# Kernel tuning notes

Hardware: AMD Instinct MI355X
Metric: run time of the kernel (lower is better)

## Reference

```python
import jax, jax.numpy as jnp
import numpy as np

H = 4096  # grid height
W = 4096  # grid width


def setup_inputs() -> dict:
    key = jax.random.key(0)
    k1, k2 = jax.random.split(key)
    x = jax.random.normal(k1, (H,), dtype=jnp.float32)
    # xavier_uniform with fan_in=3, fan_out=3 => bound = sqrt(6/(3+3)) = 1.0
    bound = float(np.sqrt(6.0 / (3.0 + 3.0)))
    w = jax.random.uniform(k2, (H, W), dtype=jnp.float32, minval=-bound, maxval=bound)
    b = jnp.zeros((H, W), dtype=jnp.float32)
    return {"x": x, "w": w, "b": b}


def _shift_down(a, k):
    # prepend k zero rows / elements along axis 0, drop last k
    pad_shape = (k,) + a.shape[1:]
    return jnp.concatenate([jnp.zeros(pad_shape, a.dtype), a[: a.shape[0] - k]], axis=0)


def reference(x, w, b):
    # The torch module zero-pads w (one row top/bottom) and keeps activation
    # rows 0 and H+1 at zero. The 3-tap stencil a[i-1],a[i],a[i+1] (padded idx)
    # for output row i reduces, in unpadded coords, to:
    #   z[i] = c[i-2]*w[i-2] + c[i-1]*w[i-1] + c[i]*w[i] + b[i]
    # with zero boundary for negative indices.
    Hh, Ww = b.shape
    wm2 = _shift_down(w, 2)  # w[i-2] with zero boundary, (H, W)
    wm1 = _shift_down(w, 1)  # w[i-1]
    # scan across columns (width); carry the activation column (H,)
    xs = (wm2.T, wm1.T, w.T, b.T)  # each (W, H)

    def step(col, ws):
        a2, a1, a0, bj = ws
        z = _shift_down(col, 2) * a2 + _shift_down(col, 1) * a1 + col * a0 + bj
        new = jnp.sin(z)
        return new, None

    final, _ = jax.lax.scan(step, x.reshape(Hh), xs)
    return final.reshape(1, Hh)
```

## Files before the change

### kernel.cpp

```cpp
#include <hip/hip_runtime.h>
#include <math.h>

#define HH 4096
#define WW 4096
#define NB 64
#define U 8
#define NGR (WW / U)
#define GATE 64


__device__ __forceinline__ unsigned long long halo_ld(unsigned long long* p) {
    return __hip_atomic_load(p, __ATOMIC_RELAXED, __HIP_MEMORY_SCOPE_AGENT);
}
__device__ __forceinline__ void halo_st(unsigned long long* p, unsigned long long v) {
    __hip_atomic_store(p, v, __ATOMIC_RELAXED, __HIP_MEMORY_SCOPE_AGENT);
}

__device__ __forceinline__ float f4c(const float4& v, int k) {
    return (k == 0) ? v.x : ((k == 1) ? v.y : ((k == 2) ? v.z : v.w));
}

__device__ __forceinline__ float wave_shr1(float src, float fill) {
    return __int_as_float(__builtin_amdgcn_update_dpp(
        __float_as_int(fill), __float_as_int(src), 0x138, 0xF, 0xF, false));
}

__device__ __forceinline__ float fast_sin(float z) {
    return __builtin_amdgcn_sinf(z * 0.15915494309189535f);
}

#define COLSTEP(M, K)                                                        \
    do {                                                                     \
        float am1 = wave_shr1(a, Hhi[M][K]);                                 \
        float am2 = wave_shr1(am1, Hlo[M][K]);                               \
        const float z = fmaf(am2, f4c(W2v[M][(K) >> 2], (K) & 3),            \
                        fmaf(am1, f4c(W1v[M][(K) >> 2], (K) & 3),            \
                        fmaf(a,   f4c(Wv[M][(K) >> 2],  (K) & 3),            \
                                  f4c(Bv[M][(K) >> 2],  (K) & 3))));         \
        a = fast_sin(z);                                                     \
        Pv[K] = a;                    \
    } while (0)

#define PUBG(JB)                                                             \
    do {                                                                     \
        float pv = 0.0f;                                                     \
        _Pragma("unroll")                                                    \
        for (int k = 0; k < U; ++k) {                                        \
            float t = __shfl(Pv[k], 62 + (lane & 1));                        \
            if ((lane >> 1) == k) pv = t;                                    \
        }                                                                    \
        const int e = (JB) + 1 + (lane >> 1);                                \
        if (lane < 16 && e < WW) {                                           \
            unsigned long long v =                                           \
                ((unsigned long long)(unsigned)(e + 1) << 32) |              \
                (unsigned long long)__float_as_uint(pv);                     \
            halo_st(&hme[(size_t)e * 2 + (lane & 1)], v);                    \
        }                                                                    \
    } while (0)

#define LOADW(M, J)                                                          \
    do {                                                                     \
        const int _j = (J);                                                  \
        Wv[M][0]  = *(const float4*)(wp  + _j);                              \
        Wv[M][1]  = *(const float4*)(wp  + _j + 4);                          \
        W1v[M][0] = *(const float4*)(wp1 + _j);                              \
        W1v[M][1] = *(const float4*)(wp1 + _j + 4);                          \
        W2v[M][0] = *(const float4*)(wp2 + _j);                              \
        W2v[M][1] = *(const float4*)(wp2 + _j + 4);                          \
        Bv[M][0]  = *(const float4*)(bp  + _j);                              \
        Bv[M][1]  = *(const float4*)(bp  + _j + 4);                          \
    } while (0)

#define UNPACKG(GIDX, BUF, SLOT)                                             \
    do {                                                                     \
        const int _jn = (GIDX) * U;                                          \
        if (blk > 0) {                                                       \
            bool myok = (lane >= 16) ||                                      \
                ((unsigned)(Hg[SLOT] >> 32) ==                               \
                 (unsigned)(_jn + (lane >> 1) + 1));                         \
            if (__builtin_expect(!__all(myok), 0)) {                         \
                for (;;) {                                                   \
                    if (lane < 16)                                           \
                        Hg[SLOT] = halo_ld(&hsrc[(size_t)_jn * 2 + lane]);   \
                    myok = (lane >= 16) ||                                   \
                        ((unsigned)(Hg[SLOT] >> 32) ==                       \
                         (unsigned)(_jn + (lane >> 1) + 1));                 \
                    if (__all(myok)) break;                                  \
                    __builtin_amdgcn_s_sleep(2);                             \
                }                                                            \
            }                                                                \
            float _hv = __uint_as_float((unsigned)(Hg[SLOT] & 0xffffffffu)); \
            _Pragma("unroll")                                                \
            for (int k = 0; k < U; ++k) {                                    \
                Hlo[BUF][k] = __shfl(_hv, 2 * k);                            \
                Hhi[BUF][k] = __shfl(_hv, 2 * k + 1);                        \
            }                                                                \
        }                                                                    \
    } while (0)

#define GROUPBODY(S)                                                         \
    do {                                                                     \
        const int G  = g4 * 4 + (S);                                         \
        const int jb = G * U;                                                \
        if (G + 1 < NGR) UNPACKG(G + 1, ((S) + 1) & 1, ((S) + 1) & 3);       \
        _Pragma("unroll")                                                    \
        for (int k = 0; k < U; ++k) COLSTEP((S) & 1, k);                     \
        PUBG(jb);                                                            \
        const int jw = jb + 2 * U;                                           \
        if (jw < WW) LOADW((S) & 1, jw);                                     \
        const int jh = jb + 4 * U;                                           \
        if (jh < WW && blk > 0 && lane < 16)                                 \
            Hg[S] = halo_ld(&hsrc[(size_t)jh * 2 + lane]);                   \
    } while (0)

__global__ __launch_bounds__(64, 1) void neural_grid_scan(
    const float* __restrict__ x, const float* __restrict__ w,
    const float* __restrict__ bb, float* __restrict__ out,
    unsigned long long* __restrict__ halo)
{
    const int lane = threadIdx.x;
    const int blk  = blockIdx.x;
    const int row  = blk * 64 + lane;
    const int r1 = (row >= 1) ? row - 1 : 0;
    const int r2 = (row >= 2) ? row - 2 : 0;

    const float* wp  = w  + (size_t)row * WW;
    const float* wp1 = w  + (size_t)r1  * WW;
    const float* wp2 = w  + (size_t)r2  * WW;
    const float* bp  = bb + (size_t)row * WW;

    unsigned long long* hme  = halo + (size_t)blk * WW * 2;
    unsigned long long* hsrc = halo + (size_t)(blk - 1) * WW * 2;

    float a = x[row];

    if (lane >= 62) {
        unsigned long long v = (1ULL << 32) | (unsigned long long)__float_as_uint(a);
        halo_st(&hme[lane - 62], v);
    }

    if (blk > 0 && lane == 0) {
        while ((unsigned)(halo_ld(&hsrc[(size_t)GATE * 2]) >> 32)
               != (unsigned)(GATE + 1)) {
            __builtin_amdgcn_s_sleep(8);
        }
    }

    float4 Wv[2][2], W1v[2][2], W2v[2][2], Bv[2][2];
    unsigned long long Hg[4];
    float Hlo[2][U] = {}, Hhi[2][U] = {};
    float Pv[U];

    LOADW(0, 0);
    LOADW(1, U);
    if (blk > 0 && lane < 16) {
        Hg[0] = halo_ld(&hsrc[(size_t)(0 * U) * 2 + lane]);
        Hg[1] = halo_ld(&hsrc[(size_t)(1 * U) * 2 + lane]);
        Hg[2] = halo_ld(&hsrc[(size_t)(2 * U) * 2 + lane]);
        Hg[3] = halo_ld(&hsrc[(size_t)(3 * U) * 2 + lane]);
    } else {
        Hg[0] = Hg[1] = Hg[2] = Hg[3] = 0;
    }
    UNPACKG(0, 0, 0);

    for (int g4 = 0; g4 < NGR / 4; ++g4) {
        GROUPBODY(0);
        GROUPBODY(1);
        GROUPBODY(2);
        GROUPBODY(3);
    }

    out[row] = a;
}

extern "C" void kernel_launch(void* const* d_in, const int* in_sizes, int n_in,
                              void* d_out, int out_size, void* d_ws, size_t ws_size,
                              hipStream_t stream) {
    const float* x = (const float*)d_in[0];
    const float* w = (const float*)d_in[1];
    const float* b = (const float*)d_in[2];
    float* out = (float*)d_out;
    unsigned long long* halo = (unsigned long long*)d_ws;
    neural_grid_scan<<<dim3(NB), dim3(64), 0, stream>>>(x, w, b, out, halo);
}
```

Before: 918.9 us.

## Batch halo polling to 32 columns per full-wave load and raise gate

Halo values from the upstream block are now fetched one 32-column batch at a time, with all 64 lanes each loading one entry, replacing per-8-column loads by 16 lanes. Readiness is checked once per batch instead of once per group, which cuts polling and the cross-lane vote work. The next batch is prefetched one batch ahead. The startup gate is raised so blocks lag further behind their producers, which lowers the chance of stalling on a batch that is not yet ready. The cost is a longer startup skew across the block chain and a dependency on data 32 columns ahead.

```diff
diff --git a/kernel.cpp b/kernel.cpp
--- a/kernel.cpp
+++ b/kernel.cpp
@@ -6,7 +6,8 @@
 #define NB 64
 #define U 8
 #define NGR (WW / U)
-#define GATE 64
+#define NBATCH (WW / 32)
+#define GATE 80
 
 
 __device__ __forceinline__ unsigned long long halo_ld(unsigned long long* p) {
@@ -71,46 +72,49 @@
         Bv[M][1]  = *(const float4*)(bp  + _j + 4);                          \
     } while (0)
 
-#define UNPACKG(GIDX, BUF, SLOT)                                             \
+#define LOADBATCH(DST, M)                                                    \
     do {                                                                     \
-        const int _jn = (GIDX) * U;                                          \
+        if (blk > 0) DST = halo_ld(&hsrc[(size_t)(M) * 64 + lane]);          \
+    } while (0)
+
+#define CHECKBATCH(REG, M)                                                   \
+    do {                                                                     \
         if (blk > 0) {                                                       \
-            bool myok = (lane >= 16) ||                                      \
-                ((unsigned)(Hg[SLOT] >> 32) ==                               \
-                 (unsigned)(_jn + (lane >> 1) + 1));                         \
-            if (__builtin_expect(!__all(myok), 0)) {                         \
+            bool ok = ((unsigned)((REG) >> 32) ==                            \
+                       (unsigned)(32 * (M) + (lane >> 1) + 1));              \
+            if (__builtin_expect(!__all(ok), 0)) {                           \
                 for (;;) {                                                   \
-                    if (lane < 16)                                           \
-                        Hg[SLOT] = halo_ld(&hsrc[(size_t)_jn * 2 + lane]);   \
-                    myok = (lane >= 16) ||                                   \
-                        ((unsigned)(Hg[SLOT] >> 32) ==                       \
-                         (unsigned)(_jn + (lane >> 1) + 1));                 \
-                    if (__all(myok)) break;                                  \
+                    REG = halo_ld(&hsrc[(size_t)(M) * 64 + lane]);           \
+                    ok = ((unsigned)((REG) >> 32) ==                         \
+                          (unsigned)(32 * (M) + (lane >> 1) + 1));           \
+                    if (__all(ok)) break;                                    \
                     __builtin_amdgcn_s_sleep(2);                             \
                 }                                                            \
-            }                                                                \
-            float _hv = __uint_as_float((unsigned)(Hg[SLOT] & 0xffffffffu)); \
-            _Pragma("unroll")                                                \
-            for (int k = 0; k < U; ++k) {                                    \
-                Hlo[BUF][k] = __shfl(_hv, 2 * k);                            \
-                Hhi[BUF][k] = __shfl(_hv, 2 * k + 1);                        \
             }                                                                \
         }                                                                    \
     } while (0)
 
-#define GROUPBODY(S)                                                         \
+#define UNPACKB(REG, I, BUF)                                                 \
     do {                                                                     \
-        const int G  = g4 * 4 + (S);                                         \
-        const int jb = G * U;                                                \
-        if (G + 1 < NGR) UNPACKG(G + 1, ((S) + 1) & 1, ((S) + 1) & 3);       \
+        if (blk > 0) {                                                       \
+            float _hv = __uint_as_float((unsigned)((REG) & 0xffffffffu));    \
+            _Pragma("unroll")                                                \
+            for (int k = 0; k < U; ++k) {                                    \
+                Hlo[BUF][k] = __shfl(_hv, 16 * (I) + 2 * k);                 \
+                Hhi[BUF][k] = __shfl(_hv, 16 * (I) + 2 * k + 1);             \
+            }                                                                \
+        }                                                                    \
+    } while (0)
+
+#define GB(S)                                                                \
+    do {                                                                     \
+        const int jb = (4 * m + (S)) * U;                                    \
+        if ((S) < 3) UNPACKB(Hga, (S) + 1, ((S) + 1) & 1);                   \
         _Pragma("unroll")                                                    \
         for (int k = 0; k < U; ++k) COLSTEP((S) & 1, k);                     \
         PUBG(jb);                                                            \
         const int jw = jb + 2 * U;                                           \
         if (jw < WW) LOADW((S) & 1, jw);                                     \
-        const int jh = jb + 4 * U;                                           \
-        if (jh < WW && blk > 0 && lane < 16)                                 \
-            Hg[S] = halo_ld(&hsrc[(size_t)jh * 2 + lane]);                   \
     } while (0)
 
 __global__ __launch_bounds__(64, 1) void neural_grid_scan(
@@ -147,27 +151,28 @@
     }
 
     float4 Wv[2][2], W1v[2][2], W2v[2][2], Bv[2][2];
-    unsigned long long Hg[4];
     float Hlo[2][U] = {}, Hhi[2][U] = {};
     float Pv[U];
+    unsigned long long Hga = 0, Hgb = 0;
 
     LOADW(0, 0);
     LOADW(1, U);
-    if (blk > 0 && lane < 16) {
-        Hg[0] = halo_ld(&hsrc[(size_t)(0 * U) * 2 + lane]);
-        Hg[1] = halo_ld(&hsrc[(size_t)(1 * U) * 2 + lane]);
-        Hg[2] = halo_ld(&hsrc[(size_t)(2 * U) * 2 + lane]);
-        Hg[3] = halo_ld(&hsrc[(size_t)(3 * U) * 2 + lane]);
-    } else {
-        Hg[0] = Hg[1] = Hg[2] = Hg[3] = 0;
-    }
-    UNPACKG(0, 0, 0);
+    LOADBATCH(Hga, 0);
+    CHECKBATCH(Hga, 0);
+    LOADBATCH(Hgb, 1);
+    UNPACKB(Hga, 0, 0);
 
-    for (int g4 = 0; g4 < NGR / 4; ++g4) {
-        GROUPBODY(0);
-        GROUPBODY(1);
-        GROUPBODY(2);
-        GROUPBODY(3);
+    for (int m = 0; m < NBATCH; ++m) {
+        GB(0);
+        GB(1);
+        GB(2);
+        GB(3);
+        if (m + 1 < NBATCH) {
+            CHECKBATCH(Hgb, m + 1);
+            Hga = Hgb;
+            if (m + 2 < NBATCH) LOADBATCH(Hgb, m + 2);
+            UNPACKB(Hga, 0, 0);
+        }
     }
 
     out[row] = a;
```

Result: slower. 972.6 us (+5.8%).

## Chain waves inside 512-thread blocks via LDS ring halos instead of global

Applied to the files above, without the earlier changes.

Switches from 64 single-wave blocks to 8 blocks of 8 waves. Within a block, neighbouring waves pass their boundary activations through per-wave LDS ring buffers, and a progress counter throttles each producer so it cannot overwrite ring slots before the consumer has read them. Only the first and last waves use the global-memory halo exchange. The goal is to cut the cross-CU atomic latency on the wavefront-pipeline critical path, at the cost of sharing CUs and adding flow-control spinning inside the block.

```diff
diff --git a/kernel.cpp b/kernel.cpp
--- a/kernel.cpp
+++ b/kernel.cpp
@@ -3,10 +3,14 @@
 
 #define HH 4096
 #define WW 4096
-#define NB 64
+#define NB 8
+#define BT 512
 #define U 8
 #define NGR (WW / U)
+#define RING_E 512
+#define RMASK (RING_E - 1)
 #define GATE 64
+#define LGATE 32
 
 
 __device__ __forceinline__ unsigned long long halo_ld(unsigned long long* p) {
@@ -14,6 +18,18 @@
 }
 __device__ __forceinline__ void halo_st(unsigned long long* p, unsigned long long v) {
     __hip_atomic_store(p, v, __ATOMIC_RELAXED, __HIP_MEMORY_SCOPE_AGENT);
+}
+__device__ __forceinline__ unsigned long long lds_ld(const unsigned long long* p) {
+    return __hip_atomic_load(p, __ATOMIC_RELAXED, __HIP_MEMORY_SCOPE_WORKGROUP);
+}
+__device__ __forceinline__ void lds_st(unsigned long long* p, unsigned long long v) {
+    __hip_atomic_store(p, v, __ATOMIC_RELAXED, __HIP_MEMORY_SCOPE_WORKGROUP);
+}
+__device__ __forceinline__ unsigned prog_ld(const unsigned* p) {
+    return __hip_atomic_load(p, __ATOMIC_RELAXED, __HIP_MEMORY_SCOPE_WORKGROUP);
+}
+__device__ __forceinline__ void prog_st(unsigned* p, unsigned v) {
+    __hip_atomic_store(p, v, __ATOMIC_RELAXED, __HIP_MEMORY_SCOPE_WORKGROUP);
 }
 
 __device__ __forceinline__ float f4c(const float4& v, int k) {
@@ -38,23 +54,40 @@
                         fmaf(a,   f4c(Wv[M][(K) >> 2],  (K) & 3),            \
                                   f4c(Bv[M][(K) >> 2],  (K) & 3))));         \
         a = fast_sin(z);                                                     \
-        Pv[K] = a;                    \
-    } while (0)
-
-#define PUBG(JB)                                                             \
-    do {                                                                     \
-        float pv = 0.0f;                                                     \
+        Pv[K] = a;                                                           \
+    } while (0)
+
+#define PACKPV(PVOUT)                                                        \
+    do {                                                                     \
+        PVOUT = 0.0f;                                                        \
         _Pragma("unroll")                                                    \
         for (int k = 0; k < U; ++k) {                                        \
             float t = __shfl(Pv[k], 62 + (lane & 1));                        \
-            if ((lane >> 1) == k) pv = t;                                    \
-        }                                                                    \
+            if ((lane >> 1) == k) PVOUT = t;                                 \
+        }                                                                    \
+    } while (0)
+
+#define PUBG(JB)                                                             \
+    do {                                                                     \
+        float pv; PACKPV(pv);                                                \
         const int e = (JB) + 1 + (lane >> 1);                                \
         if (lane < 16 && e < WW) {                                           \
             unsigned long long v =                                           \
                 ((unsigned long long)(unsigned)(e + 1) << 32) |              \
                 (unsigned long long)__float_as_uint(pv);                     \
             halo_st(&hme[(size_t)e * 2 + (lane & 1)], v);                    \
+        }                                                                    \
+    } while (0)
+
+#define LDSPUB(JB)                                                           \
+    do {                                                                     \
+        float pv; PACKPV(pv);                                                \
+        const int e = (JB) + 1 + (lane >> 1);                                \
+        if (lane < 16 && e < WW) {                                           \
+            unsigned long long v =                                           \
+                ((unsigned long long)(unsigned)(e + 1) << 32) |              \
+                (unsigned long long)__float_as_uint(pv);                     \
+            lds_st(&ldsp[((e & RMASK) << 1) | (lane & 1)], v);               \
         }                                                                    \
     } while (0)
 
@@ -98,29 +131,66 @@
         }                                                                    \
     } while (0)
 
+#define LDSUNPACK(GIDX, BUF)                                                 \
+    do {                                                                     \
+        const int _jn = (GIDX) * U;                                          \
+        const int _e  = _jn + (lane >> 1);                                   \
+        unsigned long long* _p =                                             \
+            &ldsb[((_e & RMASK) << 1) | (lane & 1)];                         \
+        bool ok = (lane >= 16) ||                                            \
+                  ((unsigned)(Lga >> 32) == (unsigned)(_e + 1));             \
+        if (__builtin_expect(!__all(ok), 0)) {                               \
+            for (;;) {                                                       \
+                Lga = lds_ld(_p);                                            \
+                ok = (lane >= 16) ||                                         \
+                     ((unsigned)(Lga >> 32) == (unsigned)(_e + 1));          \
+                if (__all(ok)) break;                                        \
+                __builtin_amdgcn_s_sleep(1);                                 \
+            }                                                                \
+        }                                                                    \
+        float _hv = __uint_as_float((unsigned)(Lga & 0xffffffffu));          \
+        _Pragma("unroll")                                                    \
+        for (int k = 0; k < U; ++k) {                                        \
+            Hlo[BUF][k] = __shfl(_hv, 2 * k);                                \
+            Hhi[BUF][k] = __shfl(_hv, 2 * k + 1);                            \
+        }                                                                    \
+        Lga = Lgb;                                                           \
+        if ((GIDX) + 2 < NGR) {                                              \
+            const int _e2 = ((GIDX) + 2) * U + (lane >> 1);                  \
+            Lgb = lds_ld(&ldsb[((_e2 & RMASK) << 1) | (lane & 1)]);          \
+        }                                                                    \
+    } while (0)
+
 #define GROUPBODY(S)                                                         \
     do {                                                                     \
-        const int G  = g4 * 4 + (S);                                         \
+        const int G  = m * 4 + (S);                                          \
         const int jb = G * U;                                                \
-        if (G + 1 < NGR) UNPACKG(G + 1, ((S) + 1) & 1, ((S) + 1) & 3);       \
+        if (G + 1 < NGR) {                                                   \
+            if (wave == 0) { UNPACKG(G + 1, ((S) + 1) & 1, ((S) + 1) & 3); } \
+            else          { LDSUNPACK(G + 1, ((S) + 1) & 1); }               \
+        }                                                                    \
         _Pragma("unroll")                                                    \
         for (int k = 0; k < U; ++k) COLSTEP((S) & 1, k);                     \
-        PUBG(jb);                                                            \
+        if (wave == 7) { PUBG(jb); } else { LDSPUB(jb); }                    \
         const int jw = jb + 2 * U;                                           \
         if (jw < WW) LOADW((S) & 1, jw);                                     \
-        const int jh = jb + 4 * U;                                           \
-        if (jh < WW && blk > 0 && lane < 16)                                 \
-            Hg[S] = halo_ld(&hsrc[(size_t)jh * 2 + lane]);                   \
-    } while (0)
-
-__global__ __launch_bounds__(64, 1) void neural_grid_scan(
+        if (wave == 0) {                                                     \
+            const int jh = jb + 4 * U;                                       \
+            if (jh < WW && blk > 0 && lane < 16)                             \
+                Hg[S] = halo_ld(&hsrc[(size_t)jh * 2 + lane]);               \
+        }                                                                    \
+    } while (0)
+
+__global__ __launch_bounds__(BT, 2) void neural_grid_scan(
     const float* __restrict__ x, const float* __restrict__ w,
     const float* __restrict__ bb, float* __restrict__ out,
     unsigned long long* __restrict__ halo)
 {
-    const int lane = threadIdx.x;
+    const int tid  = threadIdx.x;
+    const int lane = tid & 63;
+    const int wave = tid >> 6;
     const int blk  = blockIdx.x;
-    const int row  = blk * 64 + lane;
+    const int row  = blk * BT + tid;
     const int r1 = (row >= 1) ? row - 1 : 0;
     const int r2 = (row >= 2) ? row - 2 : 0;
 
@@ -132,38 +202,83 @@
     unsigned long long* hme  = halo + (size_t)blk * WW * 2;
     unsigned long long* hsrc = halo + (size_t)(blk - 1) * WW * 2;
 
+    __shared__ unsigned long long lds_h[7][RING_E * 2];
+    __shared__ unsigned int lds_prog[8];
+
+    unsigned long long* ldsb = (wave > 0) ? &lds_h[wave - 1][0] : &lds_h[0][0];
+    unsigned long long* ldsp = (wave < 7) ? &lds_h[wave][0]     : &lds_h[0][0];
+
+    {
+        unsigned long long* f = &lds_h[0][0];
+        for (int i = tid; i < 7 * RING_E * 2; i += BT) f[i] = 0;
+        if (tid < 8) lds_prog[tid] = 0;
+    }
+    __syncthreads();
+
     float a = x[row];
 
     if (lane >= 62) {
-        unsigned long long v = (1ULL << 32) | (unsigned long long)__float_as_uint(a);
-        halo_st(&hme[lane - 62], v);
-    }
-
-    if (blk > 0 && lane == 0) {
-        while ((unsigned)(halo_ld(&hsrc[(size_t)GATE * 2]) >> 32)
-               != (unsigned)(GATE + 1)) {
-            __builtin_amdgcn_s_sleep(8);
+        unsigned long long v =
+            (1ULL << 32) | (unsigned long long)__float_as_uint(a);
+        if (wave < 7) lds_st(&ldsp[lane - 62], v);
+        else          halo_st(&hme[lane - 62], v);
+    }
+
+    if (wave == 0) {
+        if (blk > 0 && lane == 0) {
+            while ((unsigned)(halo_ld(&hsrc[(size_t)GATE * 2]) >> 32)
+                   != (unsigned)(GATE + 1)) {
+                __builtin_amdgcn_s_sleep(8);
+            }
+        }
+    } else if (lane == 0) {
+        while ((unsigned)(lds_ld(&ldsb[(LGATE & RMASK) << 1]) >> 32)
+               != (unsigned)(LGATE + 1)) {
+            __builtin_amdgcn_s_sleep(2);
         }
     }
 
     float4 Wv[2][2], W1v[2][2], W2v[2][2], Bv[2][2];
     unsigned long long Hg[4];
+    unsigned long long Lga = 0, Lgb = 0;
     float Hlo[2][U] = {}, Hhi[2][U] = {};
     float Pv[U];
 
     LOADW(0, 0);
     LOADW(1, U);
-    if (blk > 0 && lane < 16) {
-        Hg[0] = halo_ld(&hsrc[(size_t)(0 * U) * 2 + lane]);
-        Hg[1] = halo_ld(&hsrc[(size_t)(1 * U) * 2 + lane]);
-        Hg[2] = halo_ld(&hsrc[(size_t)(2 * U) * 2 + lane]);
-        Hg[3] = halo_ld(&hsrc[(size_t)(3 * U) * 2 + lane]);
+    if (wave == 0) {
+        if (blk > 0 && lane < 16) {
+            Hg[0] = halo_ld(&hsrc[(size_t)(0 * U) * 2 + lane]);
+            Hg[1] = halo_ld(&hsrc[(size_t)(1 * U) * 2 + lane]);
+            Hg[2] = halo_ld(&hsrc[(size_t)(2 * U) * 2 + lane]);
+            Hg[3] = halo_ld(&hsrc[(size_t)(3 * U) * 2 + lane]);
+        } else {
+            Hg[0] = Hg[1] = Hg[2] = Hg[3] = 0;
+        }
+        UNPACKG(0, 0, 0);
     } else {
         Hg[0] = Hg[1] = Hg[2] = Hg[3] = 0;
-    }
-    UNPACKG(0, 0, 0);
-
-    for (int g4 = 0; g4 < NGR / 4; ++g4) {
+        {
+            const int e0 = 0 * U + (lane >> 1);
+            const int e1 = 1 * U + (lane >> 1);
+            Lga = lds_ld(&ldsb[((e0 & RMASK) << 1) | (lane & 1)]);
+            Lgb = lds_ld(&ldsb[((e1 & RMASK) << 1) | (lane & 1)]);
+        }
+        LDSUNPACK(0, 0);
+    }
+
+    for (int m = 0; m < NGR / 4; ++m) {
+        if (wave > 0 && lane == 0) prog_st(&lds_prog[wave], (unsigned)(4 * m));
+        if (wave < 7) {
+            unsigned gp = 0;
+            if (lane == 0) gp = prog_ld(&lds_prog[wave + 1]);
+            gp = (unsigned)__shfl((int)gp, 0);
+            while ((unsigned)(4 * m) > gp + 44u) {
+                __builtin_amdgcn_s_sleep(2);
+                if (lane == 0) gp = prog_ld(&lds_prog[wave + 1]);
+                gp = (unsigned)__shfl((int)gp, 0);
+            }
+        }
         GROUPBODY(0);
         GROUPBODY(1);
         GROUPBODY(2);
@@ -181,5 +296,5 @@
     const float* b = (const float*)d_in[2];
     float* out = (float*)d_out;
     unsigned long long* halo = (unsigned long long*)d_ws;
-    neural_grid_scan<<<dim3(NB), dim3(64), 0, stream>>>(x, w, b, out, halo);
-}
+    neural_grid_scan<<<dim3(NB), dim3(BT), 0, stream>>>(x, w, b, out, halo);
+}
```

Measured after the change: 1.885 ms. +105.2%, slower.
